# Kernel optimization log

Measured on AMD Instinct MI355X. Metric: run time of the kernel, lower is better.

The kernel has to match this reference:

```python
import jax, jax.numpy as jnp
import numpy as np

B, H, W, C = 1, 48, 48, 768
NUM_HEADS = 12
HEAD_DIM = C // NUM_HEADS  # 64
EPS = 1e-6


def setup_inputs() -> dict:
    key = jax.random.key(0)
    ks = jax.random.split(key, 8)
    s = 0.02
    return {
        "x": jax.random.normal(ks[0], (B, H, W, C), jnp.float32),
        "ln1_g": jnp.ones((C,), jnp.float32),
        "ln1_b": jnp.zeros((C,), jnp.float32),
        "qkv_w": jax.random.normal(ks[1], (C, 3 * C), jnp.float32) * s,
        "qkv_b": jax.random.normal(ks[2], (3 * C,), jnp.float32) * s,
        "rel_pos_h": jax.random.normal(ks[3], (2 * H - 1, HEAD_DIM), jnp.float32) * s,
        "rel_pos_w": jax.random.normal(ks[4], (2 * W - 1, HEAD_DIM), jnp.float32) * s,
        "proj_w": jax.random.normal(ks[5], (C, C), jnp.float32) * s,
        "proj_b": jnp.zeros((C,), jnp.float32),
        "ln2_g": jnp.ones((C,), jnp.float32),
        "ln2_b": jnp.zeros((C,), jnp.float32),
        "mlp_w1": jax.random.normal(ks[6], (C, 4 * C), jnp.float32) * s,
        "mlp_b1": jnp.zeros((4 * C,), jnp.float32),
        "mlp_w2": jax.random.normal(ks[7], (4 * C, C), jnp.float32) * s,
        "mlp_b2": jnp.zeros((C,), jnp.float32),
    }


def _layernorm(x, g, b):
    m = jnp.mean(x, axis=-1, keepdims=True)
    v = jnp.mean(jnp.square(x - m), axis=-1, keepdims=True)
    return (x - m) * jax.lax.rsqrt(v + EPS) * g + b


def _get_rel_pos(size, rel_pos):
    # grid == base grid, so no interpolation; relative index table (size, size)
    idx = jnp.arange(size)[:, None] - jnp.arange(size)[None, :] + (size - 1)
    return rel_pos[idx]  # (size, size, head_dim)


def reference(x, ln1_g, ln1_b, qkv_w, qkv_b, rel_pos_h, rel_pos_w,
              proj_w, proj_b, ln2_g, ln2_b, mlp_w1, mlp_b1, mlp_w2, mlp_b2):
    N = H * W
    scale = HEAD_DIM ** -0.5

    xn = _layernorm(x, ln1_g, ln1_b)  # (B,H,W,C)
    qkv = xn.reshape(B, N, C) @ qkv_w + qkv_b  # (B,N,3C)
    qkv = qkv.reshape(B, N, 3, NUM_HEADS, HEAD_DIM)
    qkv = jnp.transpose(qkv, (2, 0, 3, 1, 4)).reshape(3, B * NUM_HEADS, N, HEAD_DIM)
    q, k, v = qkv[0], qkv[1], qkv[2]

    attn = jnp.einsum('bnd,bmd->bnm', q * scale, k)  # (B*nh, N, N)

    Rh = _get_rel_pos(H, rel_pos_h)  # (H,H,hd)
    Rw = _get_rel_pos(W, rel_pos_w)  # (W,W,hd)
    r_q = q.reshape(B * NUM_HEADS, H, W, HEAD_DIM)
    rel_h = jnp.einsum('bhwc,hkc->bhwk', r_q, Rh)  # (B*nh,H,W,H)
    rel_w = jnp.einsum('bhwc,wkc->bhwk', r_q, Rw)  # (B*nh,H,W,W)
    attn = (attn.reshape(B * NUM_HEADS, H, W, H, W)
            + rel_h[:, :, :, :, None]
            + rel_w[:, :, :, None, :]).reshape(B * NUM_HEADS, N, N)

    attn = jax.nn.softmax(attn, axis=-1)
    out = attn @ v  # (B*nh, N, hd)
    out = out.reshape(B, NUM_HEADS, H, W, HEAD_DIM)
    out = jnp.transpose(out, (0, 2, 3, 1, 4)).reshape(B, H, W, C)
    out = out @ proj_w + proj_b

    x1 = x + out
    y = _layernorm(x1, ln2_g, ln2_b)
    h = jax.nn.gelu(y @ mlp_w1 + mlp_b1, approximate=False)  # torch GELU default = exact erf
    return x1 + (h @ mlp_w2 + mlp_b2)
```

## Files before the change

### kernel.cpp

```cpp
#include <hip/hip_runtime.h>
#include <hip/hip_bf16.h>
#include <math.h>

#define NTOK 2304
#define CDIM 768

typedef __attribute__((ext_vector_type(8))) short bf16x8;
typedef __attribute__((ext_vector_type(4))) float f32x4;

#define MFMA16(a,b,c) __builtin_amdgcn_mfma_f32_16x16x32_bf16(a,b,c,0,0,0)
#define GLOAD16(g, l) __builtin_amdgcn_global_load_lds( \
    (const __attribute__((address_space(1))) void*)(g), \
    (__attribute__((address_space(3))) void*)(l), 16, 0, 0)

__device__ __forceinline__ short f2b(float f){
  __hip_bfloat16 h = __float2bfloat16(f);
  short s; __builtin_memcpy(&s, &h, 2); return s;
}
__device__ __forceinline__ float b2f(short s){
  __hip_bfloat16 h; __builtin_memcpy(&h, &s, 2); return __bfloat162float(h);
}
__device__ __forceinline__ unsigned cvtpk(float a, float b){
  unsigned r;
  asm("v_cvt_pk_bf16_f32 %0, %1, %2" : "=v"(r) : "v"(a), "v"(b));
  return r;
}
__device__ __forceinline__ float wsum(float v){
  #pragma unroll
  for (int o = 32; o > 0; o >>= 1) v += __shfl_xor(v, o);
  return v;
}

__global__ __launch_bounds__(256) void ln_kernel(const float* __restrict__ x,
    const float* __restrict__ g, const float* __restrict__ b,
    __hip_bfloat16* __restrict__ out){
  __shared__ float sm[4];
  const int row = blockIdx.x, tid = threadIdx.x;
  const float* xr = x + (size_t)row * CDIM;
  float v0 = xr[tid], v1 = xr[tid+256], v2 = xr[tid+512];
  float s = wsum(v0+v1+v2);
  if ((tid & 63)==0) sm[tid>>6] = s;
  __syncthreads();
  float mean = (sm[0]+sm[1]+sm[2]+sm[3]) * (1.0f/CDIM);
  __syncthreads();
  float d0=v0-mean, d1=v1-mean, d2=v2-mean;
  float ss = wsum(d0*d0+d1*d1+d2*d2);
  if ((tid&63)==0) sm[tid>>6] = ss;
  __syncthreads();
  float rstd = rsqrtf((sm[0]+sm[1]+sm[2]+sm[3])*(1.0f/CDIM) + 1e-6f);
  __hip_bfloat16* o = out + (size_t)row*CDIM;
  o[tid]     = __float2bfloat16(d0*rstd*g[tid]     + b[tid]);
  o[tid+256] = __float2bfloat16(d1*rstd*g[tid+256] + b[tid+256]);
  o[tid+512] = __float2bfloat16(d2*rstd*g[tid+512] + b[tid+512]);
}

__device__ __forceinline__ void wt_tile(const float* __restrict__ W,
    __hip_bfloat16* __restrict__ Wt, int K, int N, int tx, int ty,
    float (*t)[33], int tid){
  const int n0 = tx*32, k0 = ty*32;
  const int c = tid & 31, r0 = tid >> 5;
  #pragma unroll
  for (int i = 0; i < 4; ++i){
    int r = r0 + i*8;
    t[r][c] = W[(size_t)(k0 + r)*N + n0 + c];
  }
  __syncthreads();
  #pragma unroll
  for (int i = 0; i < 4; ++i){
    int r = r0 + i*8;
    Wt[(size_t)(n0 + r)*K + k0 + c] = __float2bfloat16(t[c][r]);
  }
}

__global__ __launch_bounds__(256) void prep_kernel(
    const float* __restrict__ qkv_w, const float* __restrict__ proj_w,
    const float* __restrict__ m1w, const float* __restrict__ m2w,
    const float* __restrict__ rph, const float* __restrict__ rpw,
    __hip_bfloat16* __restrict__ qkvT, __hip_bfloat16* __restrict__ projT,
    __hip_bfloat16* __restrict__ m1T, __hip_bfloat16* __restrict__ m2T,
    __hip_bfloat16* __restrict__ rphb, __hip_bfloat16* __restrict__ rpwb){
  __shared__ float t[32][33];
  int id = blockIdx.x, tid = threadIdx.x;
  if (id < 1728)      wt_tile(qkv_w, qkvT, 768, 2304, id%72, id/72, t, tid);
  else if (id < 2304){ id -= 1728; wt_tile(proj_w, projT, 768, 768, id%24, id/24, t, tid); }
  else if (id < 4608){ id -= 2304; wt_tile(m1w, m1T, 768, 3072, id%96, id/96, t, tid); }
  else if (id < 6912){ id -= 4608; wt_tile(m2w, m2T, 3072, 768, id%24, id/24, t, tid); }
  else {
    int i = (id - 6912)*256 + tid;
    if (i < 95*64){ rphb[i] = __float2bfloat16(rph[i]); rpwb[i] = __float2bfloat16(rpw[i]); }
  }
}

__global__ __launch_bounds__(256) void vt_kernel(const __hip_bfloat16* __restrict__ qkvb,
    __hip_bfloat16* __restrict__ Vtg){
  __shared__ __hip_bfloat16 t[32][33];
  const int n0 = blockIdx.x*32, d0 = blockIdx.y*32, h = blockIdx.z;
  const int c = threadIdx.x & 31, r0 = threadIdx.x >> 5;
  #pragma unroll
  for (int i = 0; i < 4; ++i){
    int r = r0 + i*8;
    t[r][c] = qkvb[(size_t)(n0+r)*NTOK + 1536 + h*64 + d0 + c];
  }
  __syncthreads();
  #pragma unroll
  for (int i = 0; i < 4; ++i){
    int r = r0 + i*8;
    Vtg[((size_t)h*64 + d0 + r)*NTOK + n0 + c] = t[c][r];
  }
}

template<int ACT, int PARTIAL>
__global__ __launch_bounds__(256) void gemm_bf16(
    const __hip_bfloat16* __restrict__ A, const __hip_bfloat16* __restrict__ Bt,
    const float* __restrict__ bias, void* __restrict__ Cout,
    int M, int K, int N, int kst){
  __shared__ short As[2][128*32];
  __shared__ short Bs[2][128*32];
  const int tid = threadIdx.x;
  const int w = tid >> 6, lane = tid & 63;
  const int wr = w >> 1, wc = w & 1;
  const int bm = blockIdx.y*128, bn = blockIdx.x*128;
  const int kbase = blockIdx.z * kst * 32;
  const int l15 = lane & 15, l4 = lane >> 4;
  f32x4 acc[4][4] = {};

  const int ra = wr*64 + l15;
  const int rb = wc*64 + l15;
  const int kswa = l4 ^ ((ra>>1)&3);
  const int kswb = l4 ^ ((rb>>1)&3);

  auto STAGE = [&](int buf, int k0){
    #pragma unroll
    for (int r = 0; r < 4; ++r){
      if (r < 2){
        int e = r*256 + tid;
        int row = e >> 2, s = e & 3, gs = s ^ ((row>>1)&3);
        GLOAD16(A + (size_t)(bm+row)*K + k0 + gs*8, (char*)As[buf] + (r*256 + w*64)*16);
      } else {
        int e = (r-2)*256 + tid;
        int row = e >> 2, s = e & 3, gs = s ^ ((row>>1)&3);
        GLOAD16(Bt + (size_t)(bn+row)*K + k0 + gs*8, (char*)Bs[buf] + ((r-2)*256 + w*64)*16);
      }
    }
  };

  STAGE(0, kbase);
  __syncthreads();
  int cur = 0;
  for (int t = 0; t < kst; ++t){
    if (t+1 < kst) STAGE(cur^1, kbase + (t+1)*32);
    bf16x8 af[4], bfr[4];
    #pragma unroll
    for (int m = 0; m < 4; ++m)
      af[m] = *(const bf16x8*)((const char*)As[cur] + (ra + m*16)*64 + kswa*16);
    #pragma unroll
    for (int n = 0; n < 4; ++n)
      bfr[n] = *(const bf16x8*)((const char*)Bs[cur] + (rb + n*16)*64 + kswb*16);
    #pragma unroll
    for (int m = 0; m < 4; ++m)
      #pragma unroll
      for (int n = 0; n < 4; ++n)
        acc[m][n] = MFMA16(af[m], bfr[n], acc[m][n]);
    __syncthreads();
    cur ^= 1;
  }

  const int crow = bm + wr*64 + l4*4;
  const int ccol = bn + wc*64 + l15;
  float* Cp = (float*)Cout + (size_t)blockIdx.z*M*N;
  #pragma unroll
  for (int m = 0; m < 4; ++m){
    #pragma unroll
    for (int n = 0; n < 4; ++n){
      #pragma unroll
      for (int r = 0; r < 4; ++r){
        int rr = crow + m*16 + r, cc = ccol + n*16;
        if (PARTIAL){
          Cp[(size_t)rr*N + cc] = acc[m][n][r];
        } else {
          float v = acc[m][n][r] + bias[cc];
          if (ACT == 1) v = 0.5f * v * (1.0f + erff(v * 0.70710678118654752f));
          ((__hip_bfloat16*)Cout)[(size_t)rr*N + cc] = __float2bfloat16(v);
        }
      }
    }
  }
}

__global__ __launch_bounds__(256) void attn_mfma(
    const __hip_bfloat16* __restrict__ qkvb,
    const __hip_bfloat16* __restrict__ Vtg,
    const __hip_bfloat16* __restrict__ rphb,
    const __hip_bfloat16* __restrict__ rpwb,
    __hip_bfloat16* __restrict__ Opart,
    float2* __restrict__ ml){
  __shared__ short KV[2][64*64];
  __shared__ short rlh_l[4][16][16];
  __shared__ unsigned p_lds[4][16][32];

  short* Ks = KV[0];
  short* Vs = KV[1];
  short* rlt_sh = &KV[0][0];

  const int tid = threadIdx.x;
  const int w = tid >> 6, lane = tid & 63;
  const int head = blockIdx.y;
  const int part = blockIdx.z;
  const int n0 = blockIdx.x * 64;
  const int qbase = n0 + w*16;
  const int hq = qbase / 48;
  const int wq0 = qbase % 48;
  const int q = lane & 15, g = lane >> 4;

  bf16x8 qf[2];
  {
    const __hip_bfloat16* qp = qkvb + (size_t)(qbase + q)*NTOK + head*64 + g*8;
    #pragma unroll
    for (int ks = 0; ks < 2; ++ks){
      bf16x8 t = *(const bf16x8*)(qp + 32*ks);
      #pragma unroll
      for (int j = 0; j < 8; ++j) t[j] = f2b(b2f(t[j]) * 0.125f);
      qf[ks] = t;
    }
  }

  {
    int grow = hq - (part*16 + q) + 47;
    f32x4 c = {};
    #pragma unroll
    for (int ks = 0; ks < 2; ++ks){
      bf16x8 a = *(const bf16x8*)(rphb + grow*64 + g*8 + 32*ks);
      c = MFMA16(a, qf[ks], c);
    }
    #pragma unroll
    for (int r = 0; r < 4; ++r) rlh_l[w][q][g*4 + r] = f2b(c[r] * 8.0f);
  }
  #pragma unroll
  for (int f = 0; f < 4; ++f){
    int grow = wq0 + 62 - (f*16 + q);
    if (grow < 0) grow = 0;
    f32x4 c = {};
    #pragma unroll
    for (int ks = 0; ks < 2; ++ks){
      bf16x8 a = *(const bf16x8*)(rpwb + grow*64 + g*8 + 32*ks);
      c = MFMA16(a, qf[ks], c);
    }
    #pragma unroll
    for (int r = 0; r < 4; ++r)
      rlt_sh[w*1056 + q*66 + f*16 + g*4 + r] = f2b(c[r] * 8.0f);
  }
  float rlt_reg[4][3];
  #pragma unroll
  for (int r = 0; r < 4; ++r)
    #pragma unroll
    for (int j = 0; j < 3; ++j)
      rlt_reg[r][j] = b2f(rlt_sh[w*1056 + q*66 + (g*4+r) + 16*j - q + 15]);

  __syncthreads();

  float m_run = -1e30f, l_run = 0.f;
  f32x4 oacc[4] = {};

  const __hip_bfloat16* kgbase = qkvb + 768 + head*64;
  const __hip_bfloat16* vgbase = Vtg + (size_t)head*64*NTOK;
  char* prow = (char*)&p_lds[w][q][0];
  const int qs = q & 7;

  #pragma unroll
  for (int ci = 0; ci < 12; ++ci){
    const int ch = part*12 + ci;
    #pragma unroll
    for (int i = 0; i < 2; ++i){
      int e = i*256 + tid;
      int row = e >> 3, s = e & 7;
      int e0 = i*256 + w*64;
      GLOAD16(kgbase + (size_t)(ch*64 + row)*NTOK + (s ^ (row & 7))*8, (char*)Ks + e0*16);
      GLOAD16(vgbase + (size_t)row*NTOK + ch*64 + (s ^ (row & 7))*8,   (char*)Vs + e0*16);
    }
    __syncthreads();

    f32x4 st[4];
    #pragma unroll
    for (int kf = 0; kf < 4; ++kf){
      int key = kf*16 + q;
      f32x4 c = {};
      #pragma unroll
      for (int ks = 0; ks < 2; ++ks){
        int slot = (4*ks + g) ^ qs;
        bf16x8 kf8 = *(const bf16x8*)((const char*)Ks + key*128 + slot*16);
        c = MFMA16(kf8, qf[ks], c);
      }
      st[kf] = c;
    }

    float sv[4][4];
    #pragma unroll
    for (int kf = 0; kf < 4; ++kf){
      const int m = (4*ci + kf) % 3;
      const int hloc = (4*ci + kf - m) / 3;
      float rh = b2f(rlh_l[w][q][hloc]);
      #pragma unroll
      for (int r = 0; r < 4; ++r)
        sv[kf][r] = st[kf][r] + rh + rlt_reg[r][m];
    }

    float cmax = -1e30f;
    #pragma unroll
    for (int kf = 0; kf < 4; ++kf)
      #pragma unroll
      for (int r = 0; r < 4; ++r) cmax = fmaxf(cmax, sv[kf][r]);
    cmax = fmaxf(cmax, __shfl_xor(cmax, 16));
    cmax = fmaxf(cmax, __shfl_xor(cmax, 32));
    float fs = 1.0f;
    if (__any(cmax > m_run + 8.0f)){
      float nm = fmaxf(m_run, cmax);
      fs = __expf(m_run - nm);
      m_run = nm;
      float fr[4];
      #pragma unroll
      for (int r = 0; r < 4; ++r) fr[r] = __shfl(fs, g*4 + r);
      #pragma unroll
      for (int df = 0; df < 4; ++df)
        #pragma unroll
        for (int r = 0; r < 4; ++r) oacc[df][r] *= fr[r];
    }
    float p[4][4]; float lsum = 0.f;
    #pragma unroll
    for (int kf = 0; kf < 4; ++kf)
      #pragma unroll
      for (int r = 0; r < 4; ++r){ p[kf][r] = __expf(sv[kf][r] - m_run); lsum += p[kf][r]; }
    lsum += __shfl_xor(lsum, 16);
    lsum += __shfl_xor(lsum, 32);
    l_run = l_run * fs + lsum;

    #pragma unroll
    for (int kf = 0; kf < 4; ++kf){
      unsigned lo = cvtpk(p[kf][0], p[kf][1]);
      unsigned hi = cvtpk(p[kf][2], p[kf][3]);
      *(uint2*)(prow + (((2*kf + (g>>1)) ^ qs) << 4) + ((g&1) << 3)) = make_uint2(lo, hi);
    }
    #pragma unroll
    for (int ks = 0; ks < 2; ++ks){
      bf16x8 pa = *(const bf16x8*)(prow + (((4*ks + g) ^ qs) << 4));
      #pragma unroll
      for (int df = 0; df < 4; ++df){
        int d = df*16 + q;
        int slot = (4*ks + g) ^ qs;
        bf16x8 vf8 = *(const bf16x8*)((const char*)Vs + d*128 + slot*16);
        oacc[df] = MFMA16(pa, vf8, oacc[df]);
      }
    }
    __syncthreads();
  }

  __hip_bfloat16* op = Opart + (size_t)part*NTOK*CDIM;
  #pragma unroll
  for (int df = 0; df < 4; ++df)
    #pragma unroll
    for (int r = 0; r < 4; ++r)
      op[(size_t)(qbase + g*4 + r)*CDIM + head*64 + df*16 + q] =
          __float2bfloat16(oacc[df][r]);
  if (g == 0)
    ml[(size_t)part*12*NTOK + head*NTOK + qbase + q] = make_float2(m_run, l_run);
}

__global__ __launch_bounds__(256) void merge_attn(
    const __hip_bfloat16* __restrict__ Opart, const float2* __restrict__ ml,
    __hip_bfloat16* __restrict__ attb){
  const int n = blockIdx.x, tid = threadIdx.x;
  #pragma unroll
  for (int j = 0; j < 3; ++j){
    int c = tid + j*256;
    int h = c >> 6;
    float2 a = ml[h*NTOK + n];
    float2 b = ml[12*NTOK + h*NTOK + n];
    float2 d = ml[2*12*NTOK + h*NTOK + n];
    float M = fmaxf(a.x, fmaxf(b.x, d.x));
    float e0 = __expf(a.x - M), e1 = __expf(b.x - M), e2 = __expf(d.x - M);
    float L = a.y*e0 + b.y*e1 + d.y*e2;
    float o0 = __bfloat162float(Opart[(size_t)n*CDIM + c]);
    float o1 = __bfloat162float(Opart[(size_t)NTOK*CDIM + n*CDIM + c]);
    float o2 = __bfloat162float(Opart[(size_t)2*NTOK*CDIM + n*CDIM + c]);
    attb[(size_t)n*CDIM + c] = __float2bfloat16((o0*e0 + o1*e1 + o2*e2) / L);
  }
}

__global__ __launch_bounds__(256) void merge_proj_ln(
    const float* __restrict__ x, const float* __restrict__ Cp,
    const float* __restrict__ pb,
    const float* __restrict__ g2, const float* __restrict__ b2,
    __hip_bfloat16* __restrict__ x1b, __hip_bfloat16* __restrict__ yb){
  __shared__ float sm[4];
  const int row = blockIdx.x, tid = threadIdx.x;
  float v[3];
  #pragma unroll
  for (int j = 0; j < 3; ++j){
    int c = tid + j*256;
    size_t o = (size_t)row*CDIM + c;
    float s = x[o] + pb[c];
    s += Cp[o] + Cp[(size_t)NTOK*CDIM + o] + Cp[(size_t)2*NTOK*CDIM + o];
    v[j] = s;
    x1b[o] = __float2bfloat16(s);
  }
  float s = wsum(v[0]+v[1]+v[2]);
  if ((tid & 63)==0) sm[tid>>6] = s;
  __syncthreads();
  float mean = (sm[0]+sm[1]+sm[2]+sm[3]) * (1.0f/CDIM);
  __syncthreads();
  float d0=v[0]-mean, d1=v[1]-mean, d2=v[2]-mean;
  float ss = wsum(d0*d0+d1*d1+d2*d2);
  if ((tid&63)==0) sm[tid>>6] = ss;
  __syncthreads();
  float rstd = rsqrtf((sm[0]+sm[1]+sm[2]+sm[3])*(1.0f/CDIM) + 1e-6f);
  __hip_bfloat16* o = yb + (size_t)row*CDIM;
  o[tid]     = __float2bfloat16(d0*rstd*g2[tid]     + b2[tid]);
  o[tid+256] = __float2bfloat16(d1*rstd*g2[tid+256] + b2[tid+256]);
  o[tid+512] = __float2bfloat16(d2*rstd*g2[tid+512] + b2[tid+512]);
}

__global__ __launch_bounds__(256) void merge_mlp2(
    const __hip_bfloat16* __restrict__ x1b, const float* __restrict__ Cp,
    const float* __restrict__ bias, float* __restrict__ out){
  const int row = blockIdx.x, tid = threadIdx.x;
  #pragma unroll
  for (int j = 0; j < 3; ++j){
    int c = tid + j*256;
    size_t o = (size_t)row*CDIM + c;
    float s = __bfloat162float(x1b[o]) + bias[c];
    s += Cp[o] + Cp[(size_t)NTOK*CDIM + o] + Cp[(size_t)2*NTOK*CDIM + o];
    out[o] = s;
  }
}

extern "C" void kernel_launch(void* const* d_in, const int* in_sizes, int n_in,
                              void* d_out, int out_size, void* d_ws, size_t ws_size,
                              hipStream_t stream) {
  const float* x      = (const float*)d_in[0];
  const float* ln1_g  = (const float*)d_in[1];
  const float* ln1_b  = (const float*)d_in[2];
  const float* qkv_w  = (const float*)d_in[3];
  const float* qkv_b  = (const float*)d_in[4];
  const float* rph    = (const float*)d_in[5];
  const float* rpw    = (const float*)d_in[6];
  const float* proj_w = (const float*)d_in[7];
  const float* proj_b = (const float*)d_in[8];
  const float* ln2_g  = (const float*)d_in[9];
  const float* ln2_b  = (const float*)d_in[10];
  const float* mlp_w1 = (const float*)d_in[11];
  const float* mlp_b1 = (const float*)d_in[12];
  const float* mlp_w2 = (const float*)d_in[13];
  const float* mlp_b2 = (const float*)d_in[14];

  char* ws = (char*)d_ws;
  __hip_bfloat16* x1b   = (__hip_bfloat16*)(ws);
  __hip_bfloat16* m2T   = (__hip_bfloat16*)(ws + 3538944);
  __hip_bfloat16* hb    = (__hip_bfloat16*)(ws + 8257536);
  __hip_bfloat16* qkvb  = (__hip_bfloat16*)(ws + 8257536);
  __hip_bfloat16* Opart = (__hip_bfloat16*)(ws + 18874368);
  float*          Cpp   = (float*)         (ws + 8257536);
  float*          Cpm   = (float*)         (ws + 22413312);
  float2*         mlbuf = (float2*)        (ws + 29491200);
  __hip_bfloat16* Vtg   = (__hip_bfloat16*)(ws + 30154752);
  __hip_bfloat16* qkvT  = (__hip_bfloat16*)(ws + 33693696);
  __hip_bfloat16* attb  = (__hip_bfloat16*)(ws + 33693696);
  __hip_bfloat16* projT = (__hip_bfloat16*)(ws + 37232640);
  __hip_bfloat16* m1T   = (__hip_bfloat16*)(ws + 38412288);
  __hip_bfloat16* rphb  = (__hip_bfloat16*)(ws + 43646976);
  __hip_bfloat16* rpwb  = (__hip_bfloat16*)(ws + 43659136);
  __hip_bfloat16* yb    = (__hip_bfloat16*)(ws + 43671296);

  prep_kernel<<<6936, 256, 0, stream>>>(qkv_w, proj_w, mlp_w1, mlp_w2, rph, rpw,
                                        qkvT, projT, m1T, m2T, rphb, rpwb);
  ln_kernel<<<NTOK, 256, 0, stream>>>(x, ln1_g, ln1_b, yb);

  gemm_bf16<0,0><<<dim3(18, 18), 256, 0, stream>>>(
      yb, qkvT, qkv_b, qkvb, NTOK, 768, 2304, 24);

  vt_kernel<<<dim3(72, 2, 12), 256, 0, stream>>>(qkvb, Vtg);
  attn_mfma<<<dim3(36, 12, 3), 256, 0, stream>>>(qkvb, Vtg, rphb, rpwb, Opart, mlbuf);
  merge_attn<<<NTOK, 256, 0, stream>>>(Opart, mlbuf, attb);

  gemm_bf16<0,1><<<dim3(6, 18, 3), 256, 0, stream>>>(
      attb, projT, nullptr, Cpp, NTOK, 768, 768, 8);
  merge_proj_ln<<<NTOK, 256, 0, stream>>>(x, Cpp, proj_b, ln2_g, ln2_b, x1b, yb);

  gemm_bf16<1,0><<<dim3(24, 18), 256, 0, stream>>>(
      yb, m1T, mlp_b1, hb, NTOK, 768, 3072, 24);

  gemm_bf16<0,1><<<dim3(6, 18, 3), 256, 0, stream>>>(
      hb, m2T, nullptr, Cpm, NTOK, 3072, 768, 32);
  merge_mlp2<<<NTOK, 256, 0, stream>>>(x1b, Cpm, mlp_b2, (float*)d_out);
}
```

Measured before the change: 264.4 us.

## Fuse LN1 into prep, shrink GEMM N-tile, double-buffer attention KV, rebalance split-K

LayerNorm1 now runs as extra blocks inside the weight-prep kernel, which removes one launch. The GEMM block tile drops from 128x128 to 128x64, doubling grid size so the 256 CUs stay busier. The attention kernel double-buffers its K/V LDS tiles, so the next chunk loads while the current one computes, and one barrier per iteration goes away. The projection GEMM switches from 3-way to 2-way split-K with a matching merge. The cost is more LDS in attention, which may lower occupancy, and less operand reuse per GEMM block.

```diff
diff --git a/kernel.cpp b/kernel.cpp
--- a/kernel.cpp
+++ b/kernel.cpp
@@ -29,29 +29,6 @@
   #pragma unroll
   for (int o = 32; o > 0; o >>= 1) v += __shfl_xor(v, o);
   return v;
-}
-
-__global__ __launch_bounds__(256) void ln_kernel(const float* __restrict__ x,
-    const float* __restrict__ g, const float* __restrict__ b,
-    __hip_bfloat16* __restrict__ out){
-  __shared__ float sm[4];
-  const int row = blockIdx.x, tid = threadIdx.x;
-  const float* xr = x + (size_t)row * CDIM;
-  float v0 = xr[tid], v1 = xr[tid+256], v2 = xr[tid+512];
-  float s = wsum(v0+v1+v2);
-  if ((tid & 63)==0) sm[tid>>6] = s;
-  __syncthreads();
-  float mean = (sm[0]+sm[1]+sm[2]+sm[3]) * (1.0f/CDIM);
-  __syncthreads();
-  float d0=v0-mean, d1=v1-mean, d2=v2-mean;
-  float ss = wsum(d0*d0+d1*d1+d2*d2);
-  if ((tid&63)==0) sm[tid>>6] = ss;
-  __syncthreads();
-  float rstd = rsqrtf((sm[0]+sm[1]+sm[2]+sm[3])*(1.0f/CDIM) + 1e-6f);
-  __hip_bfloat16* o = out + (size_t)row*CDIM;
-  o[tid]     = __float2bfloat16(d0*rstd*g[tid]     + b[tid]);
-  o[tid+256] = __float2bfloat16(d1*rstd*g[tid+256] + b[tid+256]);
-  o[tid+512] = __float2bfloat16(d2*rstd*g[tid+512] + b[tid+512]);
 }
 
 __device__ __forceinline__ void wt_tile(const float* __restrict__ W,
@@ -72,22 +49,48 @@
   }
 }
 
+__device__ __forceinline__ void ln_row(const float* __restrict__ xr,
+    const float* __restrict__ g, const float* __restrict__ b,
+    __hip_bfloat16* __restrict__ o, float* sm, int tid){
+  float v0 = xr[tid], v1 = xr[tid+256], v2 = xr[tid+512];
+  float s = wsum(v0+v1+v2);
+  if ((tid & 63)==0) sm[tid>>6] = s;
+  __syncthreads();
+  float mean = (sm[0]+sm[1]+sm[2]+sm[3]) * (1.0f/CDIM);
+  __syncthreads();
+  float d0=v0-mean, d1=v1-mean, d2=v2-mean;
+  float ss = wsum(d0*d0+d1*d1+d2*d2);
+  if ((tid&63)==0) sm[tid>>6] = ss;
+  __syncthreads();
+  float rstd = rsqrtf((sm[0]+sm[1]+sm[2]+sm[3])*(1.0f/CDIM) + 1e-6f);
+  o[tid]     = __float2bfloat16(d0*rstd*g[tid]     + b[tid]);
+  o[tid+256] = __float2bfloat16(d1*rstd*g[tid+256] + b[tid+256]);
+  o[tid+512] = __float2bfloat16(d2*rstd*g[tid+512] + b[tid+512]);
+}
+
 __global__ __launch_bounds__(256) void prep_kernel(
     const float* __restrict__ qkv_w, const float* __restrict__ proj_w,
     const float* __restrict__ m1w, const float* __restrict__ m2w,
     const float* __restrict__ rph, const float* __restrict__ rpw,
+    const float* __restrict__ x, const float* __restrict__ ln1_g,
+    const float* __restrict__ ln1_b,
     __hip_bfloat16* __restrict__ qkvT, __hip_bfloat16* __restrict__ projT,
     __hip_bfloat16* __restrict__ m1T, __hip_bfloat16* __restrict__ m2T,
-    __hip_bfloat16* __restrict__ rphb, __hip_bfloat16* __restrict__ rpwb){
+    __hip_bfloat16* __restrict__ rphb, __hip_bfloat16* __restrict__ rpwb,
+    __hip_bfloat16* __restrict__ yb){
   __shared__ float t[32][33];
+  __shared__ float sm[4];
   int id = blockIdx.x, tid = threadIdx.x;
   if (id < 1728)      wt_tile(qkv_w, qkvT, 768, 2304, id%72, id/72, t, tid);
   else if (id < 2304){ id -= 1728; wt_tile(proj_w, projT, 768, 768, id%24, id/24, t, tid); }
   else if (id < 4608){ id -= 2304; wt_tile(m1w, m1T, 768, 3072, id%96, id/96, t, tid); }
   else if (id < 6912){ id -= 4608; wt_tile(m2w, m2T, 3072, 768, id%24, id/24, t, tid); }
-  else {
+  else if (id < 6936){
     int i = (id - 6912)*256 + tid;
     if (i < 95*64){ rphb[i] = __float2bfloat16(rph[i]); rpwb[i] = __float2bfloat16(rpw[i]); }
+  } else {
+    int row = id - 6936;
+    ln_row(x + (size_t)row*CDIM, ln1_g, ln1_b, yb + (size_t)row*CDIM, sm, tid);
   }
 }
 
@@ -115,31 +118,31 @@
     const float* __restrict__ bias, void* __restrict__ Cout,
     int M, int K, int N, int kst){
   __shared__ short As[2][128*32];
-  __shared__ short Bs[2][128*32];
+  __shared__ short Bs[2][64*32];
   const int tid = threadIdx.x;
   const int w = tid >> 6, lane = tid & 63;
   const int wr = w >> 1, wc = w & 1;
-  const int bm = blockIdx.y*128, bn = blockIdx.x*128;
+  const int bm = blockIdx.y*128, bn = blockIdx.x*64;
   const int kbase = blockIdx.z * kst * 32;
   const int l15 = lane & 15, l4 = lane >> 4;
-  f32x4 acc[4][4] = {};
+  f32x4 acc[4][2] = {};
 
   const int ra = wr*64 + l15;
-  const int rb = wc*64 + l15;
+  const int rb = wc*32 + l15;
   const int kswa = l4 ^ ((ra>>1)&3);
   const int kswb = l4 ^ ((rb>>1)&3);
 
   auto STAGE = [&](int buf, int k0){
     #pragma unroll
-    for (int r = 0; r < 4; ++r){
+    for (int r = 0; r < 3; ++r){
       if (r < 2){
         int e = r*256 + tid;
         int row = e >> 2, s = e & 3, gs = s ^ ((row>>1)&3);
-        GLOAD16(A + (size_t)(bm+row)*K + k0 + gs*8, (char*)As[buf] + (r*256 + w*64)*16);
+        GLOAD16(A + (size_t)(bm+row)*K + k0 + gs*8, (char*)As[buf] + ((r*256 + w*64)<<4));
       } else {
-        int e = (r-2)*256 + tid;
+        int e = tid;
         int row = e >> 2, s = e & 3, gs = s ^ ((row>>1)&3);
-        GLOAD16(Bt + (size_t)(bn+row)*K + k0 + gs*8, (char*)Bs[buf] + ((r-2)*256 + w*64)*16);
+        GLOAD16(Bt + (size_t)(bn+row)*K + k0 + gs*8, (char*)Bs[buf] + ((w*64)<<4));
       }
     }
   };
@@ -149,29 +152,29 @@
   int cur = 0;
   for (int t = 0; t < kst; ++t){
     if (t+1 < kst) STAGE(cur^1, kbase + (t+1)*32);
-    bf16x8 af[4], bfr[4];
+    bf16x8 af[4], bfr[2];
     #pragma unroll
     for (int m = 0; m < 4; ++m)
       af[m] = *(const bf16x8*)((const char*)As[cur] + (ra + m*16)*64 + kswa*16);
     #pragma unroll
-    for (int n = 0; n < 4; ++n)
+    for (int n = 0; n < 2; ++n)
       bfr[n] = *(const bf16x8*)((const char*)Bs[cur] + (rb + n*16)*64 + kswb*16);
     #pragma unroll
     for (int m = 0; m < 4; ++m)
       #pragma unroll
-      for (int n = 0; n < 4; ++n)
+      for (int n = 0; n < 2; ++n)
         acc[m][n] = MFMA16(af[m], bfr[n], acc[m][n]);
     __syncthreads();
     cur ^= 1;
   }
 
   const int crow = bm + wr*64 + l4*4;
-  const int ccol = bn + wc*64 + l15;
+  const int ccol = bn + wc*32 + l15;
   float* Cp = (float*)Cout + (size_t)blockIdx.z*M*N;
   #pragma unroll
   for (int m = 0; m < 4; ++m){
     #pragma unroll
-    for (int n = 0; n < 4; ++n){
+    for (int n = 0; n < 2; ++n){
       #pragma unroll
       for (int r = 0; r < 4; ++r){
         int rr = crow + m*16 + r, cc = ccol + n*16;
@@ -194,13 +197,11 @@
     const __hip_bfloat16* __restrict__ rpwb,
     __hip_bfloat16* __restrict__ Opart,
     float2* __restrict__ ml){
-  __shared__ short KV[2][64*64];
+  __shared__ short KVbuf[4][64*64];
   __shared__ short rlh_l[4][16][16];
   __shared__ unsigned p_lds[4][16][32];
 
-  short* Ks = KV[0];
-  short* Vs = KV[1];
-  short* rlt_sh = &KV[0][0];
+  short* rlt_sh = &KVbuf[0][0];
 
   const int tid = threadIdx.x;
   const int w = tid >> 6, lane = tid & 63;
@@ -266,18 +267,27 @@
   char* prow = (char*)&p_lds[w][q][0];
   const int qs = q & 7;
 
-  #pragma unroll
-  for (int ci = 0; ci < 12; ++ci){
-    const int ch = part*12 + ci;
+  auto STAGE_KV = [&](int buf, int ch){
     #pragma unroll
     for (int i = 0; i < 2; ++i){
       int e = i*256 + tid;
       int row = e >> 3, s = e & 7;
       int e0 = i*256 + w*64;
-      GLOAD16(kgbase + (size_t)(ch*64 + row)*NTOK + (s ^ (row & 7))*8, (char*)Ks + e0*16);
-      GLOAD16(vgbase + (size_t)row*NTOK + ch*64 + (s ^ (row & 7))*8,   (char*)Vs + e0*16);
-    }
+      GLOAD16(kgbase + (size_t)(ch*64 + row)*NTOK + (s ^ (row & 7))*8,
+              (char*)KVbuf[buf] + e0*16);
+      GLOAD16(vgbase + (size_t)row*NTOK + ch*64 + (s ^ (row & 7))*8,
+              (char*)KVbuf[2+buf] + e0*16);
+    }
+  };
+
+  STAGE_KV(0, part*12);
+  int cur = 0;
+  #pragma unroll
+  for (int ci = 0; ci < 12; ++ci){
     __syncthreads();
+    if (ci+1 < 12) STAGE_KV(cur^1, part*12 + ci + 1);
+    const short* Ks = KVbuf[cur];
+    const short* Vs = KVbuf[2+cur];
 
     f32x4 st[4];
     #pragma unroll
@@ -350,7 +360,7 @@
         oacc[df] = MFMA16(pa, vf8, oacc[df]);
       }
     }
-    __syncthreads();
+    cur ^= 1;
   }
 
   __hip_bfloat16* op = Opart + (size_t)part*NTOK*CDIM;
@@ -398,7 +408,7 @@
     int c = tid + j*256;
     size_t o = (size_t)row*CDIM + c;
     float s = x[o] + pb[c];
-    s += Cp[o] + Cp[(size_t)NTOK*CDIM + o] + Cp[(size_t)2*NTOK*CDIM + o];
+    s += Cp[o] + Cp[(size_t)NTOK*CDIM + o];
     v[j] = s;
     x1b[o] = __float2bfloat16(s);
   }
@@ -469,25 +479,25 @@
   __hip_bfloat16* rpwb  = (__hip_bfloat16*)(ws + 43659136);
   __hip_bfloat16* yb    = (__hip_bfloat16*)(ws + 43671296);
 
-  prep_kernel<<<6936, 256, 0, stream>>>(qkv_w, proj_w, mlp_w1, mlp_w2, rph, rpw,
-                                        qkvT, projT, m1T, m2T, rphb, rpwb);
-  ln_kernel<<<NTOK, 256, 0, stream>>>(x, ln1_g, ln1_b, yb);
-
-  gemm_bf16<0,0><<<dim3(18, 18), 256, 0, stream>>>(
+  prep_kernel<<<9240, 256, 0, stream>>>(qkv_w, proj_w, mlp_w1, mlp_w2, rph, rpw,
+                                        x, ln1_g, ln1_b,
+                                        qkvT, projT, m1T, m2T, rphb, rpwb, yb);
+
+  gemm_bf16<0,0><<<dim3(36, 18), 256, 0, stream>>>(
       yb, qkvT, qkv_b, qkvb, NTOK, 768, 2304, 24);
 
   vt_kernel<<<dim3(72, 2, 12), 256, 0, stream>>>(qkvb, Vtg);
   attn_mfma<<<dim3(36, 12, 3), 256, 0, stream>>>(qkvb, Vtg, rphb, rpwb, Opart, mlbuf);
   merge_attn<<<NTOK, 256, 0, stream>>>(Opart, mlbuf, attb);
 
-  gemm_bf16<0,1><<<dim3(6, 18, 3), 256, 0, stream>>>(
-      attb, projT, nullptr, Cpp, NTOK, 768, 768, 8);
+  gemm_bf16<0,1><<<dim3(12, 18, 2), 256, 0, stream>>>(
+      attb, projT, nullptr, Cpp, NTOK, 768, 768, 12);
   merge_proj_ln<<<NTOK, 256, 0, stream>>>(x, Cpp, proj_b, ln2_g, ln2_b, x1b, yb);
 
-  gemm_bf16<1,0><<<dim3(24, 18), 256, 0, stream>>>(
+  gemm_bf16<1,0><<<dim3(48, 18), 256, 0, stream>>>(
       yb, m1T, mlp_b1, hb, NTOK, 768, 3072, 24);
 
-  gemm_bf16<0,1><<<dim3(6, 18, 3), 256, 0, stream>>>(
+  gemm_bf16<0,1><<<dim3(12, 18, 3), 256, 0, stream>>>(
       hb, m2T, nullptr, Cpm, NTOK, 3072, 768, 32);
   merge_mlp2<<<NTOK, 256, 0, stream>>>(x1b, Cpm, mlp_b2, (float*)d_out);
 }
```

Result: faster. 255.3 us (-3.4%).
